# Kernel tuning notes

Hardware: AMD Instinct MI355X
Metric: run time of the kernel (lower is better)

## Reference

```python
import jax, jax.numpy as jnp
import numpy as np

SIGMA = 0.1
EPS = 1e-12

def setup_inputs() -> dict:
    key = jax.random.key(0)
    emb_org = jax.random.normal(key, (8192, 256), dtype=jnp.float32)
    return {"emb_org": emb_org}

def reference(emb_org):
    # L2-normalize rows (clamp norm at 1e-12 like torch)
    norm = jnp.clip(jnp.linalg.norm(emb_org, axis=1, keepdims=True), EPS, None)
    emb_n = emb_org / norm                      # [N, D]
    W = jnp.matmul(emb_n, emb_n.T) / SIGMA      # [N, N] cosine sim / sigma
    T = jax.nn.softmax(W, axis=1)               # row softmax
    emb_sft = jnp.matmul(T, emb_org)            # [N, D]
    return emb_sft
```

## Files before the change

kernel.cpp:

```cpp
#include <hip/hip_runtime.h>
#include <hip/hip_bf16.h>
#include <stdint.h>

#define NROWS 8192
#define DDIM  256
#define SIGMA_INV 10.0f

#define BM 64
#define BN 64
#define NSPLIT 4
#define JCHUNK (NROWS / NSPLIT)
#define NITER  (JCHUNK / BN)
#define PSTR   72
#define KCHB   1056
#define KNSZ   (32 * KCHB)

typedef __attribute__((ext_vector_type(8))) short bf16x8;
typedef __attribute__((ext_vector_type(4))) float f32x4;

__device__ inline unsigned short f2bf(float x) {
  __hip_bfloat16 h = __float2bfloat16(x);
  return *reinterpret_cast<unsigned short*>(&h);
}

__device__ inline void dma16(const void* g, void* l) {
  __builtin_amdgcn_global_load_lds(
      (const __attribute__((address_space(1))) unsigned int*)g,
      (__attribute__((address_space(3))) unsigned int*)l, 16, 0, 0);
}

__global__ __launch_bounds__(256) void normalize_k(const float* __restrict__ emb,
                                                   unsigned short* __restrict__ embn) {
  const int w = threadIdx.x >> 6, lane = threadIdx.x & 63;
  const int row = blockIdx.x * 4 + w;
  const float4* src = (const float4*)(emb + (size_t)row * DDIM);
  float4 v = src[lane];
  float ss = v.x * v.x + v.y * v.y + v.z * v.z + v.w * v.w;
  for (int off = 32; off >= 1; off >>= 1) ss += __shfl_xor(ss, off);
  const float sc = 1.0f / fmaxf(sqrtf(ss), 1e-12f);
  ushort4 o;
  o.x = f2bf(v.x * sc); o.y = f2bf(v.y * sc);
  o.z = f2bf(v.z * sc); o.w = f2bf(v.w * sc);
  ((ushort4*)(embn + (size_t)row * DDIM))[lane] = o;
}

__global__ __launch_bounds__(256) void transpose_k(const float* __restrict__ emb,
                                                   unsigned short* __restrict__ vt) {
  __shared__ float tile[64][65];
  const int r0 = blockIdx.x * 64, c0 = blockIdx.y * 64;
  const int tr = threadIdx.x >> 6, tc = threadIdx.x & 63;
  for (int i = 0; i < 16; ++i)
    tile[i * 4 + tr][tc] = emb[(size_t)(r0 + i * 4 + tr) * DDIM + c0 + tc];
  __syncthreads();
  unsigned short* dst = vt + (size_t)(r0 >> 6) * (DDIM * BN);
  for (int i = 0; i < 16; ++i)
    dst[(size_t)(c0 + i * 4 + tr) * BN + tc] = f2bf(tile[tc][i * 4 + tr]);
}

__global__ __launch_bounds__(256, 2) void fused_k(
    const unsigned short* __restrict__ embn,
    const unsigned short* __restrict__ vt,
    float* __restrict__ out,
    float* __restrict__ l_part)
{
  __shared__ char kn[2 * KNSZ];
  __shared__ unsigned short pl[BM * PSTR];

  const int tid = threadIdx.x;
  const int w = tid >> 6, lane = tid & 63;
  const int mg = w >> 1, dh = w & 1;
  const int q = lane >> 4, c = lane & 15;
  const int chunk = blockIdx.x & 3;
  const int mblk = blockIdx.x >> 2;
  const int row0 = mblk * BM + mg * 32;
  const int t0 = chunk * NITER;
  const int t1 = t0 + NITER;

  bf16x8 qa[2][8];
  for (int mt = 0; mt < 2; ++mt)
    for (int k = 0; k < 8; ++k)
      qa[mt][k] = *(const bf16x8*)(embn + (size_t)(row0 + mt * 16 + c) * DDIM + k * 32 + q * 8);

  f32x4 oacc[2][8];
  for (int mt = 0; mt < 2; ++mt)
    for (int u = 0; u < 8; ++u) oacc[mt][u] = {0.f, 0.f, 0.f, 0.f};
  float lacc[2][4] = {};

  {
    const char* src = (const char*)(embn + (size_t)t0 * BN * DDIM);
    for (int cc = 0; cc < 8; ++cc) {
      const int ch = w * 8 + cc;
      dma16(src + ch * 1024 + lane * 16, kn + ch * KCHB + lane * 16);
    }
  }

  for (int it = t0; it < t1; ++it) {
    const int bsel = (it - t0) & 1;
    const char* knb = kn + bsel * KNSZ;

    __syncthreads();

    if (it + 1 < t1) {
      const char* src = (const char*)(embn + (size_t)(it + 1) * BN * DDIM);
      char* dst = kn + (bsel ^ 1) * KNSZ;
      for (int cc = 0; cc < 8; ++cc) {
        const int ch = w * 8 + cc;
        dma16(src + ch * 1024 + lane * 16, dst + ch * KCHB + lane * 16);
      }
    }

    f32x4 sacc[2][2];
    for (int mt = 0; mt < 2; ++mt)
      for (int nt = 0; nt < 2; ++nt) sacc[mt][nt] = {0.f, 0.f, 0.f, 0.f};
    const int rb0 = (dh * 16 + (c >> 1)) * KCHB + (c & 1) * 512;
    const int rb1 = (dh * 16 + 8 + (c >> 1)) * KCHB + (c & 1) * 512;
    for (int k = 0; k < 8; ++k) {
      bf16x8 b0 = *(const bf16x8*)(knb + rb0 + k * 64 + q * 16);
      bf16x8 b1 = *(const bf16x8*)(knb + rb1 + k * 64 + q * 16);
      for (int mt = 0; mt < 2; ++mt) {
        sacc[mt][0] = __builtin_amdgcn_mfma_f32_16x16x32_bf16(qa[mt][k], b0, sacc[mt][0], 0, 0, 0);
        sacc[mt][1] = __builtin_amdgcn_mfma_f32_16x16x32_bf16(qa[mt][k], b1, sacc[mt][1], 0, 0, 0);
      }
    }

    const unsigned short* vtile = vt + (size_t)it * (DDIM * BN);
    bf16x8 vfrag[2][8];
    for (int kk = 0; kk < 2; ++kk)
      for (int u = 0; u < 8; ++u)
        vfrag[kk][u] = *(const bf16x8*)(vtile + (size_t)(dh * 128 + u * 16 + c) * BN + kk * 32 + q * 8);

    for (int mt = 0; mt < 2; ++mt)
      for (int nt = 0; nt < 2; ++nt)
        for (int r = 0; r < 4; ++r) {
          const float p = __expf(fmaf(SIGMA_INV, sacc[mt][nt][r], -SIGMA_INV));
          lacc[mt][r] += p;
          pl[(mg * 32 + mt * 16 + q * 4 + r) * PSTR + dh * 32 + nt * 16 + c] = f2bf(p);
        }

    __builtin_amdgcn_sched_barrier(0);
    asm volatile("s_waitcnt lgkmcnt(0)" ::: "memory");
    __builtin_amdgcn_sched_barrier(0);
    __builtin_amdgcn_s_barrier();
    __builtin_amdgcn_sched_barrier(0);

    for (int kk = 0; kk < 2; ++kk) {
      bf16x8 ap0 = *(const bf16x8*)(pl + (mg * 32 + c) * PSTR + kk * 32 + q * 8);
      bf16x8 ap1 = *(const bf16x8*)(pl + (mg * 32 + 16 + c) * PSTR + kk * 32 + q * 8);
      for (int u = 0; u < 8; ++u) {
        oacc[0][u] = __builtin_amdgcn_mfma_f32_16x16x32_bf16(ap0, vfrag[kk][u], oacc[0][u], 0, 0, 0);
        oacc[1][u] = __builtin_amdgcn_mfma_f32_16x16x32_bf16(ap1, vfrag[kk][u], oacc[1][u], 0, 0, 0);
      }
    }
  }

  for (int mt = 0; mt < 2; ++mt)
    for (int r = 0; r < 4; ++r) {
      float s = lacc[mt][r];
      s += __shfl_xor(s, 1); s += __shfl_xor(s, 2);
      s += __shfl_xor(s, 4); s += __shfl_xor(s, 8);
      if (c == 0)
        atomicAdd(&l_part[row0 + mt * 16 + q * 4 + r], s);
    }
  for (int mt = 0; mt < 2; ++mt)
    for (int u = 0; u < 8; ++u)
      for (int r = 0; r < 4; ++r)
        atomicAdd(&out[(size_t)(row0 + mt * 16 + q * 4 + r) * DDIM + dh * 128 + u * 16 + c],
                  oacc[mt][u][r]);
}

__global__ __launch_bounds__(256) void finalize_k(float* __restrict__ out,
                                                  const float* __restrict__ l_part) {
  const int row = blockIdx.x, t = threadIdx.x;
  out[(size_t)row * DDIM + t] /= l_part[row];
}

extern "C" void kernel_launch(void* const* d_in, const int* in_sizes, int n_in,
                              void* d_out, int out_size, void* d_ws, size_t ws_size,
                              hipStream_t stream) {
  const float* emb = (const float*)d_in[0];
  float* out = (float*)d_out;
  char* ws = (char*)d_ws;
  unsigned short* embn = (unsigned short*)ws;
  unsigned short* vt   = (unsigned short*)(ws + ((size_t)4 << 20));
  float* l_part        = (float*)(ws + ((size_t)8 << 20));

  hipMemsetAsync(out, 0, (size_t)NROWS * DDIM * sizeof(float), stream);
  hipMemsetAsync(l_part, 0, (size_t)NROWS * sizeof(float), stream);

  normalize_k<<<NROWS / 4, 256, 0, stream>>>(emb, embn);
  transpose_k<<<dim3(NROWS / 64, DDIM / 64), 256, 0, stream>>>(emb, vt);
  fused_k<<<(NROWS / BM) * NSPLIT, 256, 0, stream>>>(embn, vt, out, l_part);
  finalize_k<<<NROWS, 256, 0, stream>>>(out, l_part);
}
```

Measured before the change: 243.1 us.

## Software-pipeline PV matmul one tile behind QK and drop LDS K staging

Removes the double-buffered LDS staging of K tiles (global_load_lds DMA) and has each wave read K fragments straight from global memory. Restructures the loop so the P·V MFMA for tile i-1 runs after the QK MFMA for tile i, with P double-buffered in LDS, leaving one barrier per iteration plus an epilogue for the last tile. The aim is to overlap exp/softmax work with MFMA and cut LDS traffic and synchronisation. The risk is more global/L2 load latency from direct K reads, and dropping the 2-blocks-per-CU launch bound may change occupancy.

Result: slower. 374.3 us (+53.9%).

```diff
diff --git a/kernel.cpp b/kernel.cpp
--- a/kernel.cpp
+++ b/kernel.cpp
@@ -12,8 +12,6 @@
 #define JCHUNK (NROWS / NSPLIT)
 #define NITER  (JCHUNK / BN)
 #define PSTR   72
-#define KCHB   1056
-#define KNSZ   (32 * KCHB)
 
 typedef __attribute__((ext_vector_type(8))) short bf16x8;
 typedef __attribute__((ext_vector_type(4))) float f32x4;
@@ -21,12 +19,6 @@
 __device__ inline unsigned short f2bf(float x) {
   __hip_bfloat16 h = __float2bfloat16(x);
   return *reinterpret_cast<unsigned short*>(&h);
-}
-
-__device__ inline void dma16(const void* g, void* l) {
-  __builtin_amdgcn_global_load_lds(
-      (const __attribute__((address_space(1))) unsigned int*)g,
-      (__attribute__((address_space(3))) unsigned int*)l, 16, 0, 0);
 }
 
 __global__ __launch_bounds__(256) void normalize_k(const float* __restrict__ emb,
@@ -52,19 +44,18 @@
   for (int i = 0; i < 16; ++i)
     tile[i * 4 + tr][tc] = emb[(size_t)(r0 + i * 4 + tr) * DDIM + c0 + tc];
   __syncthreads();
-  unsigned short* dst = vt + (size_t)(r0 >> 6) * (DDIM * BN);
+  unsigned short* dst = vt + (size_t)(r0 >> 6) * (DDIM * 64);
   for (int i = 0; i < 16; ++i)
-    dst[(size_t)(c0 + i * 4 + tr) * BN + tc] = f2bf(tile[tc][i * 4 + tr]);
+    dst[(size_t)(c0 + i * 4 + tr) * 64 + tc] = f2bf(tile[tc][i * 4 + tr]);
 }
 
-__global__ __launch_bounds__(256, 2) void fused_k(
+__global__ __launch_bounds__(256) void fused_k(
     const unsigned short* __restrict__ embn,
     const unsigned short* __restrict__ vt,
     float* __restrict__ out,
     float* __restrict__ l_part)
 {
-  __shared__ char kn[2 * KNSZ];
-  __shared__ unsigned short pl[BM * PSTR];
+  __shared__ unsigned short pl[2][BM * PSTR];
 
   const int tid = threadIdx.x;
   const int w = tid >> 6, lane = tid & 63;
@@ -86,69 +77,77 @@
     for (int u = 0; u < 8; ++u) oacc[mt][u] = {0.f, 0.f, 0.f, 0.f};
   float lacc[2][4] = {};
 
-  {
-    const char* src = (const char*)(embn + (size_t)t0 * BN * DDIM);
-    for (int cc = 0; cc < 8; ++cc) {
-      const int ch = w * 8 + cc;
-      dma16(src + ch * 1024 + lane * 16, kn + ch * KCHB + lane * 16);
-    }
-  }
-
   for (int it = t0; it < t1; ++it) {
-    const int bsel = (it - t0) & 1;
-    const char* knb = kn + bsel * KNSZ;
-
-    __syncthreads();
-
-    if (it + 1 < t1) {
-      const char* src = (const char*)(embn + (size_t)(it + 1) * BN * DDIM);
-      char* dst = kn + (bsel ^ 1) * KNSZ;
-      for (int cc = 0; cc < 8; ++cc) {
-        const int ch = w * 8 + cc;
-        dma16(src + ch * 1024 + lane * 16, dst + ch * KCHB + lane * 16);
-      }
-    }
-
-    f32x4 sacc[2][2];
-    for (int mt = 0; mt < 2; ++mt)
-      for (int nt = 0; nt < 2; ++nt) sacc[mt][nt] = {0.f, 0.f, 0.f, 0.f};
-    const int rb0 = (dh * 16 + (c >> 1)) * KCHB + (c & 1) * 512;
-    const int rb1 = (dh * 16 + 8 + (c >> 1)) * KCHB + (c & 1) * 512;
-    for (int k = 0; k < 8; ++k) {
-      bf16x8 b0 = *(const bf16x8*)(knb + rb0 + k * 64 + q * 16);
-      bf16x8 b1 = *(const bf16x8*)(knb + rb1 + k * 64 + q * 16);
-      for (int mt = 0; mt < 2; ++mt) {
-        sacc[mt][0] = __builtin_amdgcn_mfma_f32_16x16x32_bf16(qa[mt][k], b0, sacc[mt][0], 0, 0, 0);
-        sacc[mt][1] = __builtin_amdgcn_mfma_f32_16x16x32_bf16(qa[mt][k], b1, sacc[mt][1], 0, 0, 0);
-      }
-    }
-
-    const unsigned short* vtile = vt + (size_t)it * (DDIM * BN);
-    bf16x8 vfrag[2][8];
-    for (int kk = 0; kk < 2; ++kk)
-      for (int u = 0; u < 8; ++u)
-        vfrag[kk][u] = *(const bf16x8*)(vtile + (size_t)(dh * 128 + u * 16 + c) * BN + kk * 32 + q * 8);
-
-    for (int mt = 0; mt < 2; ++mt)
-      for (int nt = 0; nt < 2; ++nt)
-        for (int r = 0; r < 4; ++r) {
-          const float p = __expf(fmaf(SIGMA_INV, sacc[mt][nt][r], -SIGMA_INV));
-          lacc[mt][r] += p;
-          pl[(mg * 32 + mt * 16 + q * 4 + r) * PSTR + dh * 32 + nt * 16 + c] = f2bf(p);
-        }
-
     __builtin_amdgcn_sched_barrier(0);
     asm volatile("s_waitcnt lgkmcnt(0)" ::: "memory");
     __builtin_amdgcn_sched_barrier(0);
     __builtin_amdgcn_s_barrier();
     __builtin_amdgcn_sched_barrier(0);
 
+    bf16x8 vfrag[2][8];
+    if (it > t0) {
+      const unsigned short* vtile = vt + (size_t)(it - 1) * (DDIM * BN);
+      for (int kk = 0; kk < 2; ++kk)
+        for (int u = 0; u < 8; ++u)
+          vfrag[kk][u] = *(const bf16x8*)(vtile + (size_t)(dh * 128 + u * 16 + c) * BN + kk * 32 + q * 8);
+    }
+
+    f32x4 sacc[2][2];
+    for (int mt = 0; mt < 2; ++mt)
+      for (int nt = 0; nt < 2; ++nt) sacc[mt][nt] = {0.f, 0.f, 0.f, 0.f};
+    {
+      const unsigned short* brow0 = embn + (size_t)(it * BN + dh * 32 + c) * DDIM;
+      const unsigned short* brow1 = brow0 + (size_t)16 * DDIM;
+      for (int k = 0; k < 8; ++k) {
+        bf16x8 b0 = *(const bf16x8*)(brow0 + k * 32 + q * 8);
+        bf16x8 b1 = *(const bf16x8*)(brow1 + k * 32 + q * 8);
+        for (int mt = 0; mt < 2; ++mt) {
+          sacc[mt][0] = __builtin_amdgcn_mfma_f32_16x16x32_bf16(qa[mt][k], b0, sacc[mt][0], 0, 0, 0);
+          sacc[mt][1] = __builtin_amdgcn_mfma_f32_16x16x32_bf16(qa[mt][k], b1, sacc[mt][1], 0, 0, 0);
+        }
+      }
+    }
+
+    if (it > t0) {
+      const unsigned short* plp = pl[(it + 1) & 1];
+      for (int kk = 0; kk < 2; ++kk) {
+        bf16x8 ap0 = *(const bf16x8*)(plp + (mg * 32 + c) * PSTR + kk * 32 + q * 8);
+        bf16x8 ap1 = *(const bf16x8*)(plp + (mg * 32 + 16 + c) * PSTR + kk * 32 + q * 8);
+        for (int u = 0; u < 8; ++u) {
+          oacc[0][u] = __builtin_amdgcn_mfma_f32_16x16x32_bf16(ap0, vfrag[kk][u], oacc[0][u], 0, 0, 0);
+          oacc[1][u] = __builtin_amdgcn_mfma_f32_16x16x32_bf16(ap1, vfrag[kk][u], oacc[1][u], 0, 0, 0);
+        }
+      }
+    }
+
+    {
+      unsigned short* plc = pl[it & 1];
+      for (int mt = 0; mt < 2; ++mt)
+        for (int nt = 0; nt < 2; ++nt)
+          for (int r = 0; r < 4; ++r) {
+            const float p = __expf(fmaf(SIGMA_INV, sacc[mt][nt][r], -SIGMA_INV));
+            lacc[mt][r] += p;
+            plc[(mg * 32 + mt * 16 + q * 4 + r) * PSTR + dh * 32 + nt * 16 + c] = f2bf(p);
+          }
+    }
+  }
+
+  {
+    __builtin_amdgcn_sched_barrier(0);
+    asm volatile("s_waitcnt lgkmcnt(0)" ::: "memory");
+    __builtin_amdgcn_sched_barrier(0);
+    __builtin_amdgcn_s_barrier();
+    __builtin_amdgcn_sched_barrier(0);
+
+    const unsigned short* vtile = vt + (size_t)(t1 - 1) * (DDIM * BN);
+    const unsigned short* plp = pl[(t1 - 1) & 1];
     for (int kk = 0; kk < 2; ++kk) {
-      bf16x8 ap0 = *(const bf16x8*)(pl + (mg * 32 + c) * PSTR + kk * 32 + q * 8);
-      bf16x8 ap1 = *(const bf16x8*)(pl + (mg * 32 + 16 + c) * PSTR + kk * 32 + q * 8);
+      bf16x8 ap0 = *(const bf16x8*)(plp + (mg * 32 + c) * PSTR + kk * 32 + q * 8);
+      bf16x8 ap1 = *(const bf16x8*)(plp + (mg * 32 + 16 + c) * PSTR + kk * 32 + q * 8);
       for (int u = 0; u < 8; ++u) {
-        oacc[0][u] = __builtin_amdgcn_mfma_f32_16x16x32_bf16(ap0, vfrag[kk][u], oacc[0][u], 0, 0, 0);
-        oacc[1][u] = __builtin_amdgcn_mfma_f32_16x16x32_bf16(ap1, vfrag[kk][u], oacc[1][u], 0, 0, 0);
+        bf16x8 vf = *(const bf16x8*)(vtile + (size_t)(dh * 128 + u * 16 + c) * BN + kk * 32 + q * 8);
+        oacc[0][u] = __builtin_amdgcn_mfma_f32_16x16x32_bf16(ap0, vf, oacc[0][u], 0, 0, 0);
+        oacc[1][u] = __builtin_amdgcn_mfma_f32_16x16x32_bf16(ap1, vf, oacc[1][u], 0, 0, 0);
       }
     }
   }
```
